# Performance work log

Hardware: AMD Instinct MI355X
Metric: run time of the kernel (lower is better)

Reference implementation:

```python
import jax, jax.numpy as jnp
import numpy as np

B, S, D = 2, 2048, 1024
H, DH = 16, 64
DM = 4096
NEG = 1e10


def setup_inputs() -> dict:
    key = jax.random.key(0)
    ks = jax.random.split(key, 8)
    sc = 1.0 / np.sqrt(D)
    return {
        "x": jax.random.normal(ks[0], (B, S, D), jnp.float32),
        "W_Q": jax.random.normal(ks[1], (H, DH, D), jnp.float32) * sc,
        "W_K": jax.random.normal(ks[2], (H, DH, D), jnp.float32) * sc,
        "W_V": jax.random.normal(ks[3], (H, DH, D), jnp.float32) * sc,
        "W_O": jax.random.normal(ks[4], (D, H * DH), jnp.float32) * sc,
        "W_in": jax.random.normal(ks[5], (DM, D), jnp.float32) * sc,
        "b_in": jnp.zeros((DM,), jnp.float32),
        "W_out": jax.random.normal(ks[6], (D, DM), jnp.float32) * sc,
        "b_out": jnp.zeros((D,), jnp.float32),
    }


def reference(x, W_Q, W_K, W_V, W_O, W_in, b_in, W_out, b_out):
    b, s, d = x.shape
    d_head = W_Q.shape[1]
    # --- Attention (faithful to original einsum/mask formulation) ---
    q = jnp.einsum('ihd,bpd->biph', W_Q, x)
    k = jnp.einsum('ihd,bpd->biph', W_K, x)
    v = jnp.einsum('ihd,bpd->biph', W_V, x)
    scores = jnp.einsum('biph,biqh->biqp', k, q)  # [b,i,q,p]
    # original: t.tril(scores) - 1e10 * (1 - triu(ones)) ; mask buffer is triu
    triu = jnp.triu(jnp.ones((s, s), x.dtype))
    masked = jnp.tril(scores) - NEG * (1.0 - triu)
    attn = jax.nn.softmax(masked / np.sqrt(d_head), axis=-1)
    z = jnp.einsum('biph,biqp->biqh', v, attn)          # [b,i,q,h]
    z_flat = z.transpose(0, 2, 1, 3).reshape(b, s, -1)   # b q (i h)
    attn_out = jnp.einsum('df,bqf->bqd', W_O, z_flat)
    # --- Block residual structure (as written: x = attn(x); x = x + x) ---
    mid = attn_out + attn_out
    # --- MLP ---
    pre = jnp.einsum('md,bpd->bpm', W_in, mid) + b_in
    h = jax.nn.relu(pre)
    mlp_out = jnp.einsum('dm,bpm->bpd', W_out, h) + b_out
    return mid + mlp_out
```

## Files before the change

### kernel.cpp

```cpp
#include <hip/hip_runtime.h>
#include <hip/hip_bf16.h>
#include <stdint.h>

typedef unsigned short ushort_t;
typedef __attribute__((ext_vector_type(8))) short short8;
typedef __attribute__((ext_vector_type(4))) float floatx4;

#define DEV __device__ __forceinline__

DEV ushort_t f2b(float f) {
  uint32_t x = __float_as_uint(f);
  uint32_t r = (x + 0x7FFFu + ((x >> 16) & 1u)) >> 16;
  return (ushort_t)r;
}
DEV float b2f(ushort_t u) { return __uint_as_float(((uint32_t)u) << 16); }

DEV void async16(const ushort_t* g, ushort_t* l) {
  __builtin_amdgcn_global_load_lds(
      (const __attribute__((address_space(1))) void*)g,
      (__attribute__((address_space(3))) void*)l, 16, 0, 0);
}

struct Cvt7 {
  const float* src[7];
  ushort_t* dst[7];
  float scale[7];
  unsigned start[8];
};
__global__ void cvt_all(Cvt7 a) {
  unsigned idx = blockIdx.x * blockDim.x + threadIdx.x;
  if (idx >= a.start[7]) return;
  int seg = 0;
#pragma unroll
  for (int j = 1; j < 7; j++) seg += (idx >= a.start[j]) ? 1 : 0;
  unsigned off = idx - a.start[seg];
  float sc = a.scale[seg];
  float4 v = ((const float4*)a.src[seg])[off];
  ((ushort4*)a.dst[seg])[off] =
      make_ushort4(f2b(v.x * sc), f2b(v.y * sc), f2b(v.z * sc), f2b(v.w * sc));
}

template <int MODE, int MT, int SWZ>
__launch_bounds__(256)
__global__ void gemm_bt(const ushort_t* __restrict__ A, const ushort_t* __restrict__ Bm,
                        int M, int N, int Kd, int ldk,
                        ushort_t* __restrict__ outB, float* __restrict__ outF,
                        const float* __restrict__ bias) {
  constexpr int TM = 32 * MT;
  __shared__ alignas(16) ushort_t As[TM * 64];
  __shared__ alignas(16) ushort_t Bs[128 * 64];
  const int tid = threadIdx.x;
  const int wave = tid >> 6, lane = tid & 63;
  const int wm = wave >> 1, wn = wave & 1;

  int bx, by;
  if constexpr (SWZ == 1) {
    const int f = blockIdx.x + gridDim.x * blockIdx.y;
    by = (f & 7) + 8 * (f / (8 * gridDim.x));
    bx = (f >> 3) % gridDim.x;
  } else if constexpr (SWZ == 2) {
    const int x = blockIdx.x, y = blockIdx.y;
    bx = 2 * (x & 3) + (y & 1);
    by = (y >> 1) + 32 * (x >> 2);
  } else {
    bx = blockIdx.x; by = blockIdx.y;
  }
  const int m0 = by * TM, n0 = bx * 128;
  const int kz = blockIdx.z * Kd;

  floatx4 acc[MT][4];
#pragma unroll
  for (int i = 0; i < MT; i++)
#pragma unroll
    for (int j = 0; j < 4; j++) acc[i][j] = (floatx4){0.f, 0.f, 0.f, 0.f};

  const int r8 = lane >> 3;
  const int scol = (((lane & 7) ^ (r8 & 7)) * 8);
  const ushort_t* gA = A + (size_t)(m0 + wave * (TM / 4) + r8) * ldk + kz + scol;
  const ushort_t* gB = Bm + (size_t)(n0 + wave * 32 + r8) * ldk + kz + scol;
  ushort_t* lA = As + wave * (TM / 4) * 64;
  ushort_t* lB = Bs + wave * 2048;

  const int fr = lane & 15, fq = lane >> 4;
  const int sw = fr & 7;
  const ushort_t* rdA = As + (wm * 16 * MT + fr) * 64;
  const ushort_t* rdB = Bs + (wn * 64 + fr) * 64;

  for (int k0 = 0; k0 < Kd; k0 += 64) {
#pragma unroll
    for (int j = 0; j < MT; j++) async16(gA + (size_t)j * 8 * ldk, lA + j * 512);
#pragma unroll
    for (int j = 0; j < 4; j++) async16(gB + (size_t)j * 8 * ldk, lB + j * 512);
    gA += 64; gB += 64;
    __syncthreads();
#pragma unroll
    for (int h = 0; h < 2; h++) {
      const int co = ((h * 4 + fq) ^ sw) * 8;
      short8 af[MT], bfv[4];
#pragma unroll
      for (int mt = 0; mt < MT; mt++) af[mt] = *(const short8*)(rdA + mt * 16 * 64 + co);
#pragma unroll
      for (int nt = 0; nt < 4; nt++) bfv[nt] = *(const short8*)(rdB + nt * 16 * 64 + co);
#pragma unroll
      for (int mt = 0; mt < MT; mt++)
#pragma unroll
        for (int nt = 0; nt < 4; nt++)
          acc[mt][nt] = __builtin_amdgcn_mfma_f32_16x16x32_bf16(af[mt], bfv[nt], acc[mt][nt], 0, 0, 0);
    }
    __syncthreads();
  }

  const int crow = m0 + wm * 16 * MT + (lane >> 4) * 4;
  const int ccol = n0 + wn * 64 + (lane & 15);
  const size_t zoff = (size_t)blockIdx.z * M * N;
#pragma unroll
  for (int mt = 0; mt < MT; mt++)
#pragma unroll
    for (int nt = 0; nt < 4; nt++) {
      floatx4 a = acc[mt][nt];
#pragma unroll
      for (int r = 0; r < 4; r++) {
        const int gm = crow + mt * 16 + r;
        const int gn = ccol + nt * 16;
        const size_t idx = (size_t)gm * N + gn;
        float v = a[r];
        if constexpr (MODE == 0) {
          outB[idx] = f2b(v);
        } else if constexpr (MODE == 1) {
          outB[idx] = f2b(v);
          outF[idx] = v + bias[gn];
        } else if constexpr (MODE == 2) {
          float t = v + bias[gn];
          outB[idx] = f2b(t > 0.f ? t : 0.f);
        } else {
          outF[zoff + idx] = v;
        }
      }
    }
}

template <int MODE>
__launch_bounds__(512, 2)
__global__ void gemm256(const ushort_t* __restrict__ A, const ushort_t* __restrict__ Bm,
                        int M, int N, int Kd, int ldk,
                        ushort_t* __restrict__ outB, float* __restrict__ outF,
                        const float* __restrict__ bias) {
  __shared__ alignas(16) ushort_t As[4][256 * 32];
  __shared__ alignas(16) ushort_t Bs[4][256 * 32];
  const int tid = threadIdx.x;
  const int lane = tid & 63;
  const int wave = tid >> 6;
  const int wm = wave >> 2, wn = wave & 3;

  const int gy = gridDim.y;
  int f = blockIdx.x + gridDim.x * blockIdx.y;
  {
    const int nwg = gridDim.x * gy;
    const int q = nwg >> 3, rr = nwg & 7;
    const int xcd = f & 7, ix = f >> 3;
    f = (xcd < rr ? xcd * (q + 1) : rr * (q + 1) + (xcd - rr) * q) + ix;
  }
  const int bx = f / gy, by = f - gy * bx;
  const int m0 = by * 256, n0 = bx * 256;
  const size_t kz = (size_t)blockIdx.z * Kd;

  floatx4 acc[8][4];
#pragma unroll
  for (int i = 0; i < 8; i++)
#pragma unroll
    for (int j = 0; j < 4; j++) acc[i][j] = (floatx4){0.f, 0.f, 0.f, 0.f};

  const int rloc = tid >> 2, cch = tid & 3;
  const int gcol = ((cch ^ ((rloc >> 1) & 3)) * 8);
  const ushort_t* gA = A + (size_t)(m0 + rloc) * ldk + kz + gcol;
  const ushort_t* gB = Bm + (size_t)(n0 + rloc) * ldk + kz + gcol;
  const int lofs = rloc * 32 + cch * 8;

#define STGA32(bufi, kofs)                                              \
  {                                                                     \
    async16(gA + (kofs), &As[bufi][lofs]);                              \
    async16(gA + (size_t)128 * ldk + (kofs), &As[bufi][4096 + lofs]);   \
  }
#define STGB32(bufi, kofs)                                              \
  {                                                                     \
    async16(gB + (kofs), &Bs[bufi][lofs]);                              \
    async16(gB + (size_t)128 * ldk + (kofs), &Bs[bufi][4096 + lofs]);   \
  }

  const int NT = Kd >> 5;
  STGA32(0, 0) STGB32(0, 0)
  if (NT > 1) { STGA32(1, 32) STGB32(1, 32) }
  if (NT > 2) { STGA32(2, 64) STGB32(2, 64) }
  if (NT > 2) asm volatile("s_waitcnt vmcnt(8)" ::: "memory");
  else if (NT > 1) asm volatile("s_waitcnt vmcnt(4)" ::: "memory");
  else asm volatile("s_waitcnt vmcnt(0)" ::: "memory");
  __builtin_amdgcn_s_barrier();

  const int fr = lane & 15, fq = lane >> 4;
  const int co = ((fq ^ ((fr >> 1) & 3)) * 8);
  const int aoff = (wm * 128 + fr) * 32 + co;
  const int boff = (wn * 64 + fr) * 32 + co;

  for (int kt = 0; kt < NT; ++kt) {
    const int cb = kt & 3;
    const int pb = (kt + 3) & 3;
    const int kof = (kt + 3) * 32;
    const bool sp = (kt + 3) < NT;
    const ushort_t* Ab = As[cb];
    const ushort_t* Bb = Bs[cb];
    short8 av[4], bv[4];

#pragma unroll
    for (int i = 0; i < 4; i++) av[i] = *(const short8*)(Ab + aoff + i * 512);
#pragma unroll
    for (int j = 0; j < 4; j++) bv[j] = *(const short8*)(Bb + boff + j * 512);
    if (sp) STGA32(pb, kof)
    __builtin_amdgcn_s_barrier();
    asm volatile("s_waitcnt lgkmcnt(0)" ::: "memory");
    __builtin_amdgcn_s_setprio(1);
#pragma unroll
    for (int i = 0; i < 4; i++)
#pragma unroll
      for (int j = 0; j < 4; j++)
        acc[i][j] = __builtin_amdgcn_mfma_f32_16x16x32_bf16(av[i], bv[j], acc[i][j], 0, 0, 0);
    __builtin_amdgcn_s_setprio(0);
    __builtin_amdgcn_s_barrier();

#pragma unroll
    for (int i = 0; i < 4; i++) av[i] = *(const short8*)(Ab + aoff + 2048 + i * 512);
    if (sp) STGB32(pb, kof)
    __builtin_amdgcn_s_barrier();
    asm volatile("s_waitcnt lgkmcnt(0)" ::: "memory");
    __builtin_amdgcn_s_setprio(1);
#pragma unroll
    for (int i = 0; i < 4; i++)
#pragma unroll
      for (int j = 0; j < 4; j++)
        acc[4 + i][j] = __builtin_amdgcn_mfma_f32_16x16x32_bf16(av[i], bv[j], acc[4 + i][j], 0, 0, 0);
    __builtin_amdgcn_s_setprio(0);
    if (kt + 3 < NT) asm volatile("s_waitcnt vmcnt(8)" ::: "memory");
    else if (kt + 2 < NT) asm volatile("s_waitcnt vmcnt(4)" ::: "memory");
    else asm volatile("s_waitcnt vmcnt(0)" ::: "memory");
    __builtin_amdgcn_s_barrier();
  }
#undef STGA32
#undef STGB32

  const int crow = m0 + wm * 128 + (lane >> 4) * 4;
  const int ccol = n0 + wn * 64 + (lane & 15);
#pragma unroll
  for (int mt = 0; mt < 8; mt++)
#pragma unroll
    for (int nt = 0; nt < 4; nt++) {
      floatx4 a = acc[mt][nt];
#pragma unroll
      for (int r = 0; r < 4; r++) {
        const int gm = crow + mt * 16 + r;
        const int gn = ccol + nt * 16;
        const size_t idx = (size_t)gm * N + gn;
        if constexpr (MODE == 0) {
          outB[idx] = f2b(a[r]);
        } else if constexpr (MODE == 2) {
          float t = a[r] + bias[gn];
          outB[idx] = f2b(t > 0.f ? t : 0.f);
        } else {
          outF[idx] = a[r];
        }
      }
    }
}

__launch_bounds__(256)
__global__ void reduce2(const float4* __restrict__ P, float4* __restrict__ out, int n4) {
  int i = blockIdx.x * blockDim.x + threadIdx.x;
  int st = gridDim.x * blockDim.x;
  for (; i < n4; i += st) {
    float4 a = out[i];
    float4 p0 = P[i], p1 = P[i + 1048576];
    a.x += p0.x + p1.x;
    a.y += p0.y + p1.y;
    a.z += p0.z + p1.z;
    a.w += p0.w + p1.w;
    out[i] = a;
  }
}

__launch_bounds__(256)
__global__ void attn1(const ushort_t* __restrict__ qkv,
                      float* __restrict__ eG, float* __restrict__ psumG) {
  const int c = blockIdx.x & 63;
  const int i = (blockIdx.x >> 6) & 15;
  const int b = blockIdx.x >> 10;
  const int t = threadIdx.x;
  const int sg = t >> 3, h8 = (t & 7) * 8;
  const int s = c * 32 + sg;
  const size_t rb = (size_t)b * 2048 * 3072 + (size_t)s * 3072 + i * 64 + h8;
  short8 q8 = *(const short8*)(qkv + rb);
  short8 k8 = *(const short8*)(qkv + rb + 1024);
  short8 v8 = *(const short8*)(qkv + rb + 2048);
  float d = 0.f;
  float vf[8];
#pragma unroll
  for (int j = 0; j < 8; j++) {
    float qf = b2f((ushort_t)q8[j]);
    float kf = b2f((ushort_t)k8[j]);
    vf[j] = b2f((ushort_t)v8[j]);
    d += qf * kf;
  }
  d += __shfl_xor(d, 1, 64);
  d += __shfl_xor(d, 2, 64);
  d += __shfl_xor(d, 4, 64);
  if ((t & 7) == 0) eG[((size_t)(b * 16 + i)) * 2048 + s] = __expf(d * 0.125f);
  __shared__ float vs[32][68];
#pragma unroll
  for (int j = 0; j < 8; j += 4)
    *(float4*)&vs[sg][h8 + j] = make_float4(vf[j], vf[j + 1], vf[j + 2], vf[j + 3]);
  __syncthreads();
  if (t < 64) {
    float acc = 0.f;
#pragma unroll 8
    for (int sgi = 0; sgi < 32; sgi++) acc += vs[sgi][t];
    psumG[(((size_t)(b * 16 + i)) * 64 + c) * 64 + t] = acc;
  }
}

__launch_bounds__(256)
__global__ void attn2(const ushort_t* __restrict__ qkv,
                      const float* __restrict__ eG, const float* __restrict__ psumG,
                      ushort_t* __restrict__ Z) {
  const int wave = threadIdx.x >> 6, h = threadIdx.x & 63;
  const int c = (blockIdx.x & 15) * 4 + wave;
  const int i = (blockIdx.x >> 4) & 15;
  const int b = blockIdx.x >> 8;
  const size_t rowbase = (size_t)b * 2048 * 3072;
  const size_t pbase = ((size_t)(b * 16 + i)) * 64;
  float r0 = 0.f, r1 = 0.f, r2 = 0.f, r3 = 0.f;
  {
    int cc = c + 1;
    for (; cc + 3 < 64; cc += 4) {
      r0 += psumG[(pbase + cc) * 64 + h];
      r1 += psumG[(pbase + cc + 1) * 64 + h];
      r2 += psumG[(pbase + cc + 2) * 64 + h];
      r3 += psumG[(pbase + cc + 3) * 64 + h];
    }
    for (; cc < 64; cc++) r0 += psumG[(pbase + cc) * 64 + h];
  }
  float run = (r0 + r1) + (r2 + r3);
  const size_t ebase = ((size_t)(b * 16 + i)) * 2048;
  for (int t4 = 1; t4 >= 0; t4--) {
    float vv[16], num[16], rcp[16];
#pragma unroll
    for (int j = 0; j < 16; j++) {
      const int s = c * 32 + t4 * 16 + j;
      vv[j] = b2f(qkv[rowbase + (size_t)s * 3072 + 2048 + i * 64 + h]);
      float e = eG[ebase + s];
      num[j] = e * vv[j];
      float d = e + (float)(2047 - s);
      float r = __builtin_amdgcn_rcpf(d);
      rcp[j] = r * (2.f - d * r);
    }
#pragma unroll
    for (int j = 15; j >= 0; j--) {
      const int s = c * 32 + t4 * 16 + j;
      float z = (num[j] + run) * rcp[j];
      Z[((size_t)b * 2048 + s) * 1024 + i * 64 + h] = f2b(z);
      run += vv[j];
    }
  }
}

extern "C" void kernel_launch(void* const* d_in, const int* in_sizes, int n_in,
                              void* d_out, int out_size, void* d_ws, size_t ws_size,
                              hipStream_t stream) {
  const float* x     = (const float*)d_in[0];
  const float* W_Q   = (const float*)d_in[1];
  const float* W_K   = (const float*)d_in[2];
  const float* W_V   = (const float*)d_in[3];
  const float* W_O   = (const float*)d_in[4];
  const float* W_in  = (const float*)d_in[5];
  const float* b_in  = (const float*)d_in[6];
  const float* W_out = (const float*)d_in[7];
  const float* b_out = (const float*)d_in[8];
  float* out = (float*)d_out;

  char* base = (char*)d_ws;
  const size_t MB = 1048576;
  ushort_t* Xb    = (ushort_t*)(base + 0 * MB);
  ushort_t* Wqkv  = (ushort_t*)(base + 8 * MB);
  ushort_t* WOb   = (ushort_t*)(base + 14 * MB);
  ushort_t* Z     = (ushort_t*)(base + 16 * MB);
  ushort_t* QKV   = (ushort_t*)(base + 24 * MB);
  ushort_t* midb  = (ushort_t*)(base + 48 * MB);
  ushort_t* Winb  = (ushort_t*)(base + 56 * MB);
  ushort_t* Woutb = (ushort_t*)(base + 64 * MB);
  ushort_t* Hb    = (ushort_t*)(base + 72 * MB);
  float*    P     = (float*)(base + 0 * MB);
  float*    psumG = (float*)(base + 72 * MB);
  float*    eG    = (float*)(base + 72 * MB + 524288);

  Cvt7 ca;
  ca.src[0] = x;     ca.dst[0] = Xb;               ca.scale[0] = 1.f;
  ca.src[1] = W_Q;   ca.dst[1] = Wqkv;             ca.scale[1] = 1.f;
  ca.src[2] = W_K;   ca.dst[2] = Wqkv + 1048576;   ca.scale[2] = 1.f;
  ca.src[3] = W_V;   ca.dst[3] = Wqkv + 2097152;   ca.scale[3] = 1.f;
  ca.src[4] = W_O;   ca.dst[4] = WOb;              ca.scale[4] = 2.f;
  ca.src[5] = W_in;  ca.dst[5] = Winb;             ca.scale[5] = 1.f;
  ca.src[6] = W_out; ca.dst[6] = Woutb;            ca.scale[6] = 1.f;
  unsigned n4s[7] = {1048576, 262144, 262144, 262144, 262144, 1048576, 1048576};
  unsigned acc4 = 0;
  for (int j = 0; j < 7; j++) { ca.start[j] = acc4; acc4 += n4s[j]; }
  ca.start[7] = acc4;
  cvt_all<<<dim3((acc4 + 255) / 256), dim3(256), 0, stream>>>(ca);

  gemm256<0><<<dim3(12, 16), 512, 0, stream>>>(Xb, Wqkv, 4096, 3072, 1024, 1024,
                                               QKV, nullptr, nullptr);
  attn1<<<dim3(2048), 256, 0, stream>>>(QKV, eG, psumG);
  attn2<<<dim3(512), 256, 0, stream>>>(QKV, eG, psumG, Z);
  gemm_bt<1, 2, 1><<<dim3(8, 64), 256, 0, stream>>>(Z, WOb, 4096, 1024, 1024, 1024,
                                                    midb, out, b_out);
  gemm256<2><<<dim3(16, 16), 512, 0, stream>>>(midb, Winb, 4096, 4096, 1024, 1024,
                                               Hb, nullptr, b_in);
  gemm_bt<3, 2, 2><<<dim3(8, 64, 2), 256, 0, stream>>>(Hb, Woutb, 4096, 1024, 2048, 4096,
                                                       nullptr, P, nullptr);
  reduce2<<<dim3(1024), 256, 0, stream>>>((const float4*)P, (float4*)out, 1048576);
}
```

Before: 279.8 us.

## Fuse QKV projection with q·k score and V partial-sum epilogue

The weight conversion now interleaves W_Q and W_K rows in 64-row blocks, so each 256-column tile of a new fused QKV GEMM holds matching Q and K columns for two heads. The GEMM epilogue computes the per-position q·k dot product through shared memory and writes exp scores, and for V tiles it writes V plus per-chunk column sums. This removes the full QKV store and reload and the separate attn1 kernel. The cost is a heavier epilogue in the GEMM, and the generic gemm256 loses its split-K and fp32-output paths.

```diff
diff --git a/kernel.cpp b/kernel.cpp
--- a/kernel.cpp
+++ b/kernel.cpp
@@ -25,6 +25,7 @@
   const float* src[7];
   ushort_t* dst[7];
   float scale[7];
+  int mode[7];
   unsigned start[8];
 };
 __global__ void cvt_all(Cvt7 a) {
@@ -34,9 +35,15 @@
 #pragma unroll
   for (int j = 1; j < 7; j++) seg += (idx >= a.start[j]) ? 1 : 0;
   unsigned off = idx - a.start[seg];
+  unsigned doff = off;
+  const int m = a.mode[seg];
+  if (m) {
+    unsigned row = off >> 8, col = off & 255u;
+    doff = ((((row >> 6) << 7) + (row & 63u) + (m == 2 ? 64u : 0u)) << 8) | col;
+  }
   float sc = a.scale[seg];
   float4 v = ((const float4*)a.src[seg])[off];
-  ((ushort4*)a.dst[seg])[off] =
+  ((ushort4*)a.dst[seg])[doff] =
       make_ushort4(f2b(v.x * sc), f2b(v.y * sc), f2b(v.z * sc), f2b(v.w * sc));
 }
 
@@ -162,7 +169,6 @@
   }
   const int bx = f / gy, by = f - gy * bx;
   const int m0 = by * 256, n0 = bx * 256;
-  const size_t kz = (size_t)blockIdx.z * Kd;
 
   floatx4 acc[8][4];
 #pragma unroll
@@ -172,8 +178,8 @@
 
   const int rloc = tid >> 2, cch = tid & 3;
   const int gcol = ((cch ^ ((rloc >> 1) & 3)) * 8);
-  const ushort_t* gA = A + (size_t)(m0 + rloc) * ldk + kz + gcol;
-  const ushort_t* gB = Bm + (size_t)(n0 + rloc) * ldk + kz + gcol;
+  const ushort_t* gA = A + (size_t)(m0 + rloc) * ldk + gcol;
+  const ushort_t* gB = Bm + (size_t)(n0 + rloc) * ldk + gcol;
   const int lofs = rloc * 32 + cch * 8;
 
 #define STGA32(bufi, kofs)                                              \
@@ -189,11 +195,9 @@
 
   const int NT = Kd >> 5;
   STGA32(0, 0) STGB32(0, 0)
-  if (NT > 1) { STGA32(1, 32) STGB32(1, 32) }
-  if (NT > 2) { STGA32(2, 64) STGB32(2, 64) }
-  if (NT > 2) asm volatile("s_waitcnt vmcnt(8)" ::: "memory");
-  else if (NT > 1) asm volatile("s_waitcnt vmcnt(4)" ::: "memory");
-  else asm volatile("s_waitcnt vmcnt(0)" ::: "memory");
+  STGA32(1, 32) STGB32(1, 32)
+  STGA32(2, 64) STGB32(2, 64)
+  asm volatile("s_waitcnt vmcnt(8)" ::: "memory");
   __builtin_amdgcn_s_barrier();
 
   const int fr = lane & 15, fq = lane >> 4;
@@ -258,16 +262,184 @@
         const int gm = crow + mt * 16 + r;
         const int gn = ccol + nt * 16;
         const size_t idx = (size_t)gm * N + gn;
-        if constexpr (MODE == 0) {
-          outB[idx] = f2b(a[r]);
-        } else if constexpr (MODE == 2) {
+        if constexpr (MODE == 2) {
           float t = a[r] + bias[gn];
           outB[idx] = f2b(t > 0.f ? t : 0.f);
         } else {
-          outF[idx] = a[r];
+          outB[idx] = f2b(a[r]);
         }
       }
     }
+}
+
+__launch_bounds__(512, 2)
+__global__ void qkv_fused(const ushort_t* __restrict__ A, const ushort_t* __restrict__ Bm,
+                          ushort_t* __restrict__ Vb, float* __restrict__ eG,
+                          float* __restrict__ psumG) {
+  __shared__ alignas(16) ushort_t As[4][256 * 32];
+  __shared__ alignas(16) ushort_t Bs[4][256 * 32];
+  const int ldk = 1024;
+  const int tid = threadIdx.x;
+  const int lane = tid & 63;
+  const int wave = tid >> 6;
+  const int wm = wave >> 2, wn = wave & 3;
+
+  const int gy = gridDim.y;
+  int f = blockIdx.x + gridDim.x * blockIdx.y;
+  {
+    const int nwg = gridDim.x * gy;
+    const int q = nwg >> 3, rr = nwg & 7;
+    const int xcd = f & 7, ix = f >> 3;
+    f = (xcd < rr ? xcd * (q + 1) : rr * (q + 1) + (xcd - rr) * q) + ix;
+  }
+  const int bx = f / gy, by = f - gy * bx;
+  const int m0 = by * 256, n0 = bx * 256;
+
+  floatx4 acc[8][4];
+#pragma unroll
+  for (int i = 0; i < 8; i++)
+#pragma unroll
+    for (int j = 0; j < 4; j++) acc[i][j] = (floatx4){0.f, 0.f, 0.f, 0.f};
+
+  const int rloc = tid >> 2, cch = tid & 3;
+  const int gcol = ((cch ^ ((rloc >> 1) & 3)) * 8);
+  const ushort_t* gA = A + (size_t)(m0 + rloc) * ldk + gcol;
+  const ushort_t* gB = Bm + (size_t)(n0 + rloc) * ldk + gcol;
+  const int lofs = rloc * 32 + cch * 8;
+
+#define STGA32(bufi, kofs)                                              \
+  {                                                                     \
+    async16(gA + (kofs), &As[bufi][lofs]);                              \
+    async16(gA + (size_t)128 * ldk + (kofs), &As[bufi][4096 + lofs]);   \
+  }
+#define STGB32(bufi, kofs)                                              \
+  {                                                                     \
+    async16(gB + (kofs), &Bs[bufi][lofs]);                              \
+    async16(gB + (size_t)128 * ldk + (kofs), &Bs[bufi][4096 + lofs]);   \
+  }
+
+  const int NT = 32;
+  STGA32(0, 0) STGB32(0, 0)
+  STGA32(1, 32) STGB32(1, 32)
+  STGA32(2, 64) STGB32(2, 64)
+  asm volatile("s_waitcnt vmcnt(8)" ::: "memory");
+  __builtin_amdgcn_s_barrier();
+
+  const int fr = lane & 15, fq = lane >> 4;
+  const int co = ((fq ^ ((fr >> 1) & 3)) * 8);
+  const int aoff = (wm * 128 + fr) * 32 + co;
+  const int boff = (wn * 64 + fr) * 32 + co;
+
+  for (int kt = 0; kt < NT; ++kt) {
+    const int cb = kt & 3;
+    const int pb = (kt + 3) & 3;
+    const int kof = (kt + 3) * 32;
+    const bool sp = (kt + 3) < NT;
+    const ushort_t* Ab = As[cb];
+    const ushort_t* Bb = Bs[cb];
+    short8 av[4], bv[4];
+
+#pragma unroll
+    for (int i = 0; i < 4; i++) av[i] = *(const short8*)(Ab + aoff + i * 512);
+#pragma unroll
+    for (int j = 0; j < 4; j++) bv[j] = *(const short8*)(Bb + boff + j * 512);
+    if (sp) STGA32(pb, kof)
+    __builtin_amdgcn_s_barrier();
+    asm volatile("s_waitcnt lgkmcnt(0)" ::: "memory");
+    __builtin_amdgcn_s_setprio(1);
+#pragma unroll
+    for (int i = 0; i < 4; i++)
+#pragma unroll
+      for (int j = 0; j < 4; j++)
+        acc[i][j] = __builtin_amdgcn_mfma_f32_16x16x32_bf16(av[i], bv[j], acc[i][j], 0, 0, 0);
+    __builtin_amdgcn_s_setprio(0);
+    __builtin_amdgcn_s_barrier();
+
+#pragma unroll
+    for (int i = 0; i < 4; i++) av[i] = *(const short8*)(Ab + aoff + 2048 + i * 512);
+    if (sp) STGB32(pb, kof)
+    __builtin_amdgcn_s_barrier();
+    asm volatile("s_waitcnt lgkmcnt(0)" ::: "memory");
+    __builtin_amdgcn_s_setprio(1);
+#pragma unroll
+    for (int i = 0; i < 4; i++)
+#pragma unroll
+      for (int j = 0; j < 4; j++)
+        acc[4 + i][j] = __builtin_amdgcn_mfma_f32_16x16x32_bf16(av[i], bv[j], acc[4 + i][j], 0, 0, 0);
+    __builtin_amdgcn_s_setprio(0);
+    if (kt + 3 < NT) asm volatile("s_waitcnt vmcnt(8)" ::: "memory");
+    else if (kt + 2 < NT) asm volatile("s_waitcnt vmcnt(4)" ::: "memory");
+    else asm volatile("s_waitcnt vmcnt(0)" ::: "memory");
+    __builtin_amdgcn_s_barrier();
+  }
+#undef STGA32
+#undef STGB32
+
+  const int b = m0 >> 11;
+  if (bx < 8) {
+    const int pair = wm * 2 + (wn >> 1);
+    float* epl = (pair < 2) ? ((float*)&As[0][0] + pair * 8192)
+                            : ((float*)&Bs[0][0] + (pair - 2) * 8192);
+    const int fq4 = fq * 4;
+    if (wn & 1) {
+#pragma unroll
+      for (int mt = 0; mt < 8; mt++)
+#pragma unroll
+        for (int nt = 0; nt < 4; nt++)
+#pragma unroll
+          for (int r = 0; r < 4; r++)
+            epl[(mt * 16 + fq4 + r) * 64 + nt * 16 + fr] = acc[mt][nt][r];
+    }
+    __syncthreads();
+    if (!(wn & 1)) {
+      const int head = bx * 2 + (wn >> 1);
+      const int sbase = (m0 & 2047) + wm * 128;
+      float* eOut = eG + (((size_t)(b * 16 + head)) << 11) + sbase;
+#pragma unroll
+      for (int mt = 0; mt < 8; mt++)
+#pragma unroll
+        for (int r = 0; r < 4; r++) {
+          const int rl = mt * 16 + fq4 + r;
+          float d = 0.f;
+#pragma unroll
+          for (int nt = 0; nt < 4; nt++) d += acc[mt][nt][r] * epl[rl * 64 + nt * 16 + fr];
+          d += __shfl_xor(d, 1, 64);
+          d += __shfl_xor(d, 2, 64);
+          d += __shfl_xor(d, 4, 64);
+          d += __shfl_xor(d, 8, 64);
+          if (fr == 0) eOut[rl] = __expf(d * 0.125f);
+        }
+    }
+  } else {
+    const int vcolb = (bx - 8) * 256 + wn * 64;
+    const int i = vcolb >> 6;
+    const int crow = m0 + wm * 128 + fq * 4;
+#pragma unroll
+    for (int mt = 0; mt < 8; mt++)
+#pragma unroll
+      for (int nt = 0; nt < 4; nt++) {
+        floatx4 a = acc[mt][nt];
+#pragma unroll
+        for (int r = 0; r < 4; r++)
+          Vb[(size_t)(crow + mt * 16 + r) * 1024 + vcolb + nt * 16 + fr] = f2b(a[r]);
+      }
+    const int cbase = ((m0 & 2047) >> 5) + wm * 4;
+#pragma unroll
+    for (int c2 = 0; c2 < 4; c2++)
+#pragma unroll
+      for (int nt = 0; nt < 4; nt++) {
+        float v = 0.f;
+#pragma unroll
+        for (int mtl = 0; mtl < 2; mtl++) {
+          floatx4 aa = acc[c2 * 2 + mtl][nt];
+          v += (aa[0] + aa[1]) + (aa[2] + aa[3]);
+        }
+        v += __shfl_xor(v, 16, 64);
+        v += __shfl_xor(v, 32, 64);
+        if (fq == 0)
+          psumG[(((size_t)(b * 16 + i)) * 64 + cbase + c2) * 64 + nt * 16 + fr] = v;
+      }
+  }
 }
 
 __launch_bounds__(256)
@@ -286,53 +458,13 @@
 }
 
 __launch_bounds__(256)
-__global__ void attn1(const ushort_t* __restrict__ qkv,
-                      float* __restrict__ eG, float* __restrict__ psumG) {
-  const int c = blockIdx.x & 63;
-  const int i = (blockIdx.x >> 6) & 15;
-  const int b = blockIdx.x >> 10;
-  const int t = threadIdx.x;
-  const int sg = t >> 3, h8 = (t & 7) * 8;
-  const int s = c * 32 + sg;
-  const size_t rb = (size_t)b * 2048 * 3072 + (size_t)s * 3072 + i * 64 + h8;
-  short8 q8 = *(const short8*)(qkv + rb);
-  short8 k8 = *(const short8*)(qkv + rb + 1024);
-  short8 v8 = *(const short8*)(qkv + rb + 2048);
-  float d = 0.f;
-  float vf[8];
-#pragma unroll
-  for (int j = 0; j < 8; j++) {
-    float qf = b2f((ushort_t)q8[j]);
-    float kf = b2f((ushort_t)k8[j]);
-    vf[j] = b2f((ushort_t)v8[j]);
-    d += qf * kf;
-  }
-  d += __shfl_xor(d, 1, 64);
-  d += __shfl_xor(d, 2, 64);
-  d += __shfl_xor(d, 4, 64);
-  if ((t & 7) == 0) eG[((size_t)(b * 16 + i)) * 2048 + s] = __expf(d * 0.125f);
-  __shared__ float vs[32][68];
-#pragma unroll
-  for (int j = 0; j < 8; j += 4)
-    *(float4*)&vs[sg][h8 + j] = make_float4(vf[j], vf[j + 1], vf[j + 2], vf[j + 3]);
-  __syncthreads();
-  if (t < 64) {
-    float acc = 0.f;
-#pragma unroll 8
-    for (int sgi = 0; sgi < 32; sgi++) acc += vs[sgi][t];
-    psumG[(((size_t)(b * 16 + i)) * 64 + c) * 64 + t] = acc;
-  }
-}
-
-__launch_bounds__(256)
-__global__ void attn2(const ushort_t* __restrict__ qkv,
+__global__ void attn2(const ushort_t* __restrict__ Vb,
                       const float* __restrict__ eG, const float* __restrict__ psumG,
                       ushort_t* __restrict__ Z) {
   const int wave = threadIdx.x >> 6, h = threadIdx.x & 63;
   const int c = (blockIdx.x & 15) * 4 + wave;
   const int i = (blockIdx.x >> 4) & 15;
   const int b = blockIdx.x >> 8;
-  const size_t rowbase = (size_t)b * 2048 * 3072;
   const size_t pbase = ((size_t)(b * 16 + i)) * 64;
   float r0 = 0.f, r1 = 0.f, r2 = 0.f, r3 = 0.f;
   {
@@ -352,7 +484,7 @@
 #pragma unroll
     for (int j = 0; j < 16; j++) {
       const int s = c * 32 + t4 * 16 + j;
-      vv[j] = b2f(qkv[rowbase + (size_t)s * 3072 + 2048 + i * 64 + h]);
+      vv[j] = b2f(Vb[((size_t)b * 2048 + s) * 1024 + i * 64 + h]);
       float e = eG[ebase + s];
       num[j] = e * vv[j];
       float d = e + (float)(2047 - s);
@@ -389,7 +521,7 @@
   ushort_t* Wqkv  = (ushort_t*)(base + 8 * MB);
   ushort_t* WOb   = (ushort_t*)(base + 14 * MB);
   ushort_t* Z     = (ushort_t*)(base + 16 * MB);
-  ushort_t* QKV   = (ushort_t*)(base + 24 * MB);
+  ushort_t* Vb    = (ushort_t*)(base + 24 * MB);
   ushort_t* midb  = (ushort_t*)(base + 48 * MB);
   ushort_t* Winb  = (ushort_t*)(base + 56 * MB);
   ushort_t* Woutb = (ushort_t*)(base + 64 * MB);
@@ -399,23 +531,21 @@
   float*    eG    = (float*)(base + 72 * MB + 524288);
 
   Cvt7 ca;
-  ca.src[0] = x;     ca.dst[0] = Xb;               ca.scale[0] = 1.f;
-  ca.src[1] = W_Q;   ca.dst[1] = Wqkv;             ca.scale[1] = 1.f;
-  ca.src[2] = W_K;   ca.dst[2] = Wqkv + 1048576;   ca.scale[2] = 1.f;
-  ca.src[3] = W_V;   ca.dst[3] = Wqkv + 2097152;   ca.scale[3] = 1.f;
-  ca.src[4] = W_O;   ca.dst[4] = WOb;              ca.scale[4] = 2.f;
-  ca.src[5] = W_in;  ca.dst[5] = Winb;             ca.scale[5] = 1.f;
-  ca.src[6] = W_out; ca.dst[6] = Woutb;            ca.scale[6] = 1.f;
+  ca.src[0] = x;     ca.dst[0] = Xb;               ca.scale[0] = 1.f; ca.mode[0] = 0;
+  ca.src[1] = W_Q;   ca.dst[1] = Wqkv;             ca.scale[1] = 1.f; ca.mode[1] = 1;
+  ca.src[2] = W_K;   ca.dst[2] = Wqkv;             ca.scale[2] = 1.f; ca.mode[2] = 2;
+  ca.src[3] = W_V;   ca.dst[3] = Wqkv + 2097152;   ca.scale[3] = 1.f; ca.mode[3] = 0;
+  ca.src[4] = W_O;   ca.dst[4] = WOb;              ca.scale[4] = 2.f; ca.mode[4] = 0;
+  ca.src[5] = W_in;  ca.dst[5] = Winb;             ca.scale[5] = 1.f; ca.mode[5] = 0;
+  ca.src[6] = W_out; ca.dst[6] = Woutb;            ca.scale[6] = 1.f; ca.mode[6] = 0;
   unsigned n4s[7] = {1048576, 262144, 262144, 262144, 262144, 1048576, 1048576};
   unsigned acc4 = 0;
   for (int j = 0; j < 7; j++) { ca.start[j] = acc4; acc4 += n4s[j]; }
   ca.start[7] = acc4;
   cvt_all<<<dim3((acc4 + 255) / 256), dim3(256), 0, stream>>>(ca);
 
-  gemm256<0><<<dim3(12, 16), 512, 0, stream>>>(Xb, Wqkv, 4096, 3072, 1024, 1024,
-                                               QKV, nullptr, nullptr);
-  attn1<<<dim3(2048), 256, 0, stream>>>(QKV, eG, psumG);
-  attn2<<<dim3(512), 256, 0, stream>>>(QKV, eG, psumG, Z);
+  qkv_fused<<<dim3(12, 16), 512, 0, stream>>>(Xb, Wqkv, Vb, eG, psumG);
+  attn2<<<dim3(512), 256, 0, stream>>>(Vb, eG, psumG, Z);
   gemm_bt<1, 2, 1><<<dim3(8, 64), 256, 0, stream>>>(Z, WOb, 4096, 1024, 1024, 1024,
                                                     midb, out, b_out);
   gemm256<2><<<dim3(16, 16), 512, 0, stream>>>(midb, Winb, 4096, 4096, 1024, 1024,
```

After: 282.1 us. About the same (+0.8%).
